# Kernel optimization log

Hardware: AMD Instinct MI355X
Metric: run time of the kernel (lower is better)

## Reference

```python
import jax, jax.numpy as jnp
import numpy as np

N = 64    # input_size (number of causal nodes)
H = 512   # hidden_size
M = 64    # mediate_size
B = 1024  # batched derivative evaluations (original processes one (1,N) state at a time)


def setup_inputs() -> dict:
    key = jax.random.key(0)
    ks = jax.random.split(key, 8)
    s = lambda fan_in: 1.0 / np.sqrt(fan_in)
    x = jax.random.normal(ks[0], (B, N), dtype=jnp.float32)
    # stacked per-node weights (one set per node i in 0..N-1)
    W1 = jax.random.uniform(ks[1], (N, H, N), jnp.float32, -s(N), s(N))        # net_1 layer 1, no bias
    W2 = jax.random.uniform(ks[2], (N, M, H), jnp.float32, -s(H), s(H))        # net_1 layer 2, no bias
    W3 = jax.random.uniform(ks[3], (N, H, M + N), jnp.float32, -s(M + N), s(M + N))  # net_3 layer 1
    b3 = jax.random.uniform(ks[4], (N, H), jnp.float32, -s(M + N), s(M + N))
    W4 = jax.random.uniform(ks[5], (N, H), jnp.float32, -s(H), s(H))           # net_3 layer 2 (out dim 1)
    b4 = jax.random.uniform(ks[6], (N,), jnp.float32, -s(H), s(H))
    return {"x": x, "W1": W1, "W2": W2, "W3": W3, "b3": b3, "W4": W4, "b4": b4}


def reference(x, W1, W2, W3, b3, W4, b4):
    # Faithful DAG-case CausalDerivative.forward, batched over B states and
    # grouped over the N per-node MLPs (replacing N python-loop iterations).
    eye = jnp.eye(N, dtype=x.dtype)
    inputs_1 = x[:, None, :] * (1.0 - eye)          # (B, N, N): node i sees all-but-own value
    inputs_2 = x[:, None, :] * eye                  # (B, N, N): node i sees only own value
    h1 = jax.nn.relu(jnp.einsum('bni,nhi->bnh', inputs_1, W1))   # (B, N, H)
    r1 = jax.nn.relu(jnp.einsum('bnh,nmh->bnm', h1, W2))         # (B, N, M)
    rep3 = jnp.concatenate([r1, inputs_2], axis=-1)              # (B, N, M+N)
    h3 = jax.nn.relu(jnp.einsum('bnk,nhk->bnh', rep3, W3) + b3)  # (B, N, H)
    out = jax.nn.relu(jnp.einsum('bnh,nh->bn', h3, W4) + b4)     # (B, N) derivatives
    return out
```

## Files before the change

### kernel.cpp

```cpp
#include <hip/hip_runtime.h>

#define NN 64
#define HH 512

typedef _Float16 h8 __attribute__((ext_vector_type(8)));
typedef float    fx4 __attribute__((ext_vector_type(4)));

#define MFMA __builtin_amdgcn_mfma_f32_16x16x32_f16

#define WS_NEEDED 12713984ull

typedef __attribute__((address_space(1))) const unsigned int gu32;
typedef __attribute__((address_space(3))) unsigned int       lu32;

__device__ __forceinline__ void gld16(const void* g, void* l) {
    __builtin_amdgcn_global_load_lds((gu32*)g, (lu32*)l, 16, 0, 0);
}

__device__ __forceinline__ h8 cvt8(const float* __restrict__ s) {
    float4 a = *(const float4*)s, b = *(const float4*)(s + 4);
    h8 h;
    h[0]=(_Float16)a.x; h[1]=(_Float16)a.y; h[2]=(_Float16)a.z; h[3]=(_Float16)a.w;
    h[4]=(_Float16)b.x; h[5]=(_Float16)b.y; h[6]=(_Float16)b.z; h[7]=(_Float16)b.w;
    return h;
}

__global__ __launch_bounds__(256)
void cvt_frag(const float* __restrict__ W1, const float* __restrict__ W2,
              const float* __restrict__ W3, char* __restrict__ ws)
{
    const int g    = blockIdx.x * 256 + threadIdx.x;
    const int n    = g >> 12;
    const int c    = (g >> 9) & 7;
    const int ks   = (g >> 8) & 1;
    const int nt   = (g >> 6) & 3;
    const int l    = g & 63;
    const int pos  = l & 15;
    const int quad = l >> 4;

    _Float16* o1 = (_Float16*)ws;
    _Float16* o2 = o1 + 2097152;
    _Float16* o3 = o2 + 2097152;
    float*    oc = (float*)(ws + 12582912);

    {
        const float* s = W1 + (size_t)n * 32768
                            + (size_t)(c * 64 + nt * 16 + pos) * 64
                            + ks * 32 + quad * 8;
        *(h8*)(o1 + (size_t)g * 8) = cvt8(s);
    }
    {
        const float* s = W2 + (size_t)n * 32768
                            + (size_t)(nt * 16 + pos) * 512
                            + c * 64 + ks * 32 + quad * 8;
        *(h8*)(o2 + (size_t)g * 8) = cvt8(s);
    }
    {
        const float* s = W3 + (size_t)n * 65536
                            + (size_t)(c * 64 + nt * 16 + pos) * 128
                            + ks * 32 + quad * 8;
        *(h8*)(o3 + (size_t)g * 8) = cvt8(s);
    }
    if (g < 32768) {
        const int n3 = g >> 9;
        const int h3 = g & 511;
        oc[g] = W3[(size_t)n3 * 65536 + (size_t)h3 * 128 + 64 + n3];
    }
}

__global__ __launch_bounds__(256, 2)
void causal_mfma5(const float* __restrict__ x, const char* __restrict__ ws,
                  const float* __restrict__ b3, const float* __restrict__ W4,
                  const float* __restrict__ b4, float* __restrict__ out)
{
    __shared__ __align__(16) char smem[57856];
    _Float16* w1b  = (_Float16*)smem;
    _Float16* w2b  = w1b + 8192;
    _Float16* priv = w2b + 8192;
    float*    w3cs = (float*)(smem + 51200);
    float*    b3s  = w3cs + 512;
    float*    w4s  = b3s + 512;
    float*    xns  = w4s + 512;

    const int tid  = threadIdx.x;
    const int bid  = blockIdx.x;
    const int n    = bid & 63;
    const int tile = bid >> 6;
    const int lane = tid & 63;
    const int pos  = lane & 15;
    const int quad = lane >> 4;
    const int wv   = __builtin_amdgcn_readfirstlane(tid >> 6);
    const int row0 = tile * 128;
    const int wrow = wv << 5;

    const _Float16* W1f  = (const _Float16*)ws + (size_t)n * 32768;
    const _Float16* W2f  = (const _Float16*)ws + 2097152 + (size_t)n * 32768;
    const _Float16* W3f  = (const _Float16*)ws + 4194304 + (size_t)n * 32768;
    const float*    w3cp = (const float*)(ws + 12582912) + n * 512;

    {
        const _Float16* s1 = W1f + wv * 1024 + lane * 8;
        gld16(s1,       w1b + wv * 1024);
        gld16(s1 + 512, w1b + wv * 1024 + 512);
        const _Float16* s2 = W2f + wv * 1024 + lane * 8;
        gld16(s2,       w2b + wv * 1024);
        gld16(s2 + 512, w2b + wv * 1024 + 512);
    }
    #pragma unroll
    for (int k = 0; k < 2; ++k) {
        const int h = tid + k * 256;
        w3cs[h] = w3cp[h];
        b3s[h]  = b3[n * HH + h];
        w4s[h]  = W4[n * HH + h];
    }
    if (tid < 128) xns[tid] = x[(size_t)(row0 + tid) * NN + n];

    h8 aX[2][2];
    #pragma unroll
    for (int mt = 0; mt < 2; ++mt)
        #pragma unroll
        for (int ks = 0; ks < 2; ++ks) {
            const float* p = x + (size_t)(row0 + wrow + mt * 16 + pos) * NN + ks * 32 + quad * 8;
            float4 a = *(const float4*)p, bq = *(const float4*)(p + 4);
            float v[8] = {a.x, a.y, a.z, a.w, bq.x, bq.y, bq.z, bq.w};
            const int base = ks * 32 + quad * 8;
            #pragma unroll
            for (int j = 0; j < 8; ++j) if (base + j == n) v[j] = 0.f;
            h8 h;
            #pragma unroll
            for (int j = 0; j < 8; ++j) h[j] = (_Float16)v[j];
            aX[mt][ks] = h;
        }
    __syncthreads();

    _Float16* P = priv + wv * 2304;

    fx4 acc2[2][4] = {};
    for (int c = 0; c < 8; ++c) {
        const int cb = c & 1;
        if (c < 7) {
            const _Float16* s1 = W1f + (c + 1) * 4096 + wv * 1024 + lane * 8;
            gld16(s1,       w1b + (cb ^ 1) * 4096 + wv * 1024);
            gld16(s1 + 512, w1b + (cb ^ 1) * 4096 + wv * 1024 + 512);
            const _Float16* s2 = W2f + (c + 1) * 4096 + wv * 1024 + lane * 8;
            gld16(s2,       w2b + (cb ^ 1) * 4096 + wv * 1024);
            gld16(s2 + 512, w2b + (cb ^ 1) * 4096 + wv * 1024 + 512);
        } else {
            const _Float16* s3 = W3f + wv * 1024 + lane * 8;
            gld16(s3,       w1b + wv * 1024);
            gld16(s3 + 512, w1b + wv * 1024 + 512);
        }
        const h8* F1 = (const h8*)(w1b + cb * 4096);
        fx4 accA[2][4] = {};
        #pragma unroll
        for (int ks = 0; ks < 2; ++ks)
            #pragma unroll
            for (int nt = 0; nt < 4; ++nt) {
                h8 bf = F1[(ks * 4 + nt) * 64 + lane];
                accA[0][nt] = MFMA(aX[0][ks], bf, accA[0][nt], 0, 0, 0);
                accA[1][nt] = MFMA(aX[1][ks], bf, accA[1][nt], 0, 0, 0);
            }
        #pragma unroll
        for (int mt = 0; mt < 2; ++mt)
            #pragma unroll
            for (int nt = 0; nt < 4; ++nt)
                #pragma unroll
                for (int r = 0; r < 4; ++r)
                    P[(mt * 16 + quad * 4 + r) * 72 + nt * 16 + pos] =
                        (_Float16)fmaxf(accA[mt][nt][r], 0.f);
        h8 aH[2][2];
        #pragma unroll
        for (int mt = 0; mt < 2; ++mt)
            #pragma unroll
            for (int ks = 0; ks < 2; ++ks)
                aH[mt][ks] = *(const h8*)(P + (mt * 16 + pos) * 72 + ks * 32 + quad * 8);
        const h8* F2 = (const h8*)(w2b + cb * 4096);
        #pragma unroll
        for (int ks = 0; ks < 2; ++ks)
            #pragma unroll
            for (int cm = 0; cm < 4; ++cm) {
                h8 bf = F2[(ks * 4 + cm) * 64 + lane];
                acc2[0][cm] = MFMA(aH[0][ks], bf, acc2[0][cm], 0, 0, 0);
                acc2[1][cm] = MFMA(aH[1][ks], bf, acc2[1][cm], 0, 0, 0);
            }
        __syncthreads();
    }

    #pragma unroll
    for (int mt = 0; mt < 2; ++mt)
        #pragma unroll
        for (int cm = 0; cm < 4; ++cm)
            #pragma unroll
            for (int r = 0; r < 4; ++r)
                P[(mt * 16 + quad * 4 + r) * 72 + cm * 16 + pos] =
                    (_Float16)fmaxf(acc2[mt][cm][r], 0.f);
    h8 aR[2][2];
    #pragma unroll
    for (int mt = 0; mt < 2; ++mt)
        #pragma unroll
        for (int ks = 0; ks < 2; ++ks)
            aR[mt][ks] = *(const h8*)(P + (mt * 16 + pos) * 72 + ks * 32 + quad * 8);
    h8 af3[2];
    #pragma unroll
    for (int mt = 0; mt < 2; ++mt) {
        h8 h;
        #pragma unroll
        for (int j = 0; j < 8; ++j) h[j] = (_Float16)0.f;
        if (quad == 0) { h[0] = (_Float16)xns[wrow + mt * 16 + pos]; h[1] = (_Float16)1.f; }
        af3[mt] = h;
    }

    float o[2][4] = {};
    for (int c = 0; c < 8; ++c) {
        const int cb = c & 1;
        const int hc = c << 6;
        if (c < 7) {
            const _Float16* s3 = W3f + (c + 1) * 4096 + wv * 1024 + lane * 8;
            gld16(s3,       w1b + (cb ^ 1) * 4096 + wv * 1024);
            gld16(s3 + 512, w1b + (cb ^ 1) * 4096 + wv * 1024 + 512);
        }
        const h8* F3 = (const h8*)(w1b + cb * 4096);
        fx4 acc3[2][4] = {};
        #pragma unroll
        for (int ks = 0; ks < 2; ++ks)
            #pragma unroll
            for (int nt = 0; nt < 4; ++nt) {
                h8 bf = F3[(ks * 4 + nt) * 64 + lane];
                acc3[0][nt] = MFMA(aR[0][ks], bf, acc3[0][nt], 0, 0, 0);
                acc3[1][nt] = MFMA(aR[1][ks], bf, acc3[1][nt], 0, 0, 0);
            }
        #pragma unroll
        for (int nt = 0; nt < 4; ++nt) {
            h8 bf3;
            #pragma unroll
            for (int j = 0; j < 8; ++j) bf3[j] = (_Float16)0.f;
            if (quad == 0) {
                const int h = hc + nt * 16 + pos;
                bf3[0] = (_Float16)w3cs[h];
                bf3[1] = (_Float16)b3s[h];
            }
            acc3[0][nt] = MFMA(af3[0], bf3, acc3[0][nt], 0, 0, 0);
            acc3[1][nt] = MFMA(af3[1], bf3, acc3[1][nt], 0, 0, 0);
        }
        #pragma unroll
        for (int nt = 0; nt < 4; ++nt) {
            const float w4v = w4s[hc + nt * 16 + pos];
            #pragma unroll
            for (int mt = 0; mt < 2; ++mt)
                #pragma unroll
                for (int r = 0; r < 4; ++r)
                    o[mt][r] = fmaf(fmaxf(acc3[mt][nt][r], 0.f), w4v, o[mt][r]);
        }
        __syncthreads();
    }

    #pragma unroll
    for (int m = 1; m < 16; m <<= 1)
        #pragma unroll
        for (int mt = 0; mt < 2; ++mt)
            #pragma unroll
            for (int r = 0; r < 4; ++r)
                o[mt][r] += __shfl_xor(o[mt][r], m, 64);

    if (pos == 0) {
        const float bb = b4[n];
        #pragma unroll
        for (int mt = 0; mt < 2; ++mt)
            #pragma unroll
            for (int r = 0; r < 4; ++r) {
                const int row = row0 + wrow + mt * 16 + quad * 4 + r;
                out[(size_t)row * 64 + n] = fmaxf(o[mt][r] + bb, 0.f);
            }
    }
}

__device__ __forceinline__ void cvt_store16(_Float16* d, const float4* p) {
    h8 h0, h1;
    h0[0]=(_Float16)p[0].x; h0[1]=(_Float16)p[0].y; h0[2]=(_Float16)p[0].z; h0[3]=(_Float16)p[0].w;
    h0[4]=(_Float16)p[1].x; h0[5]=(_Float16)p[1].y; h0[6]=(_Float16)p[1].z; h0[7]=(_Float16)p[1].w;
    h1[0]=(_Float16)p[2].x; h1[1]=(_Float16)p[2].y; h1[2]=(_Float16)p[2].z; h1[3]=(_Float16)p[2].w;
    h1[4]=(_Float16)p[3].x; h1[5]=(_Float16)p[3].y; h1[6]=(_Float16)p[3].z; h1[7]=(_Float16)p[3].w;
    *(h8*)d = h0; *((h8*)d + 1) = h1;
}

__global__ __launch_bounds__(256, 2)
void causal_mfma3(const float* __restrict__ x,  const float* __restrict__ W1,
                  const float* __restrict__ W2, const float* __restrict__ W3,
                  const float* __restrict__ b3, const float* __restrict__ W4,
                  const float* __restrict__ b4, float* __restrict__ out)
{
    __shared__ __align__(16) char smem[61952];
    _Float16* W1c  = (_Float16*)smem;
    _Float16* W2c  = W1c + 2 * 4608;
    _Float16* priv = W2c + 2 * 4608;
    float*    w3cs = (float*)(smem + 55296);
    float*    b3s  = w3cs + 512;
    float*    w4s  = b3s + 512;
    float*    xns  = w4s + 512;

    const int tid  = threadIdx.x;
    const int bid  = blockIdx.x;
    const int n    = bid & 63;
    const int tile = bid >> 6;
    const int lane = tid & 63;
    const int pos  = lane & 15;
    const int quad = lane >> 4;
    const int wv   = __builtin_amdgcn_readfirstlane(tid >> 6);
    const int row0 = tile * 128;
    const int wrow = wv << 5;

    const float* W1n = W1 + (size_t)n * HH * NN;
    const float* W2n = W2 + (size_t)n * NN * HH;
    const float* W3n = W3 + (size_t)n * HH * 128;

    const int trow = tid >> 2;
    const int tcol = (tid & 3) << 4;

    {
        float4 p1[4], p2[4];
        #pragma unroll
        for (int q = 0; q < 4; ++q) p1[q] = *(const float4*)(W1n + trow * 64 + tcol + q * 4);
        #pragma unroll
        for (int q = 0; q < 4; ++q) p2[q] = *(const float4*)(W2n + (size_t)trow * HH + tcol + q * 4);
        #pragma unroll
        for (int k = 0; k < 2; ++k) {
            const int h = tid + k * 256;
            w3cs[h] = W3n[(size_t)h * 128 + 64 + n];
            b3s[h]  = b3[n * HH + h];
            w4s[h]  = W4[n * HH + h];
        }
        if (tid < 128) xns[tid] = x[(size_t)(row0 + tid) * NN + n];
        cvt_store16(W1c + trow * 72 + tcol, p1);
        cvt_store16(W2c + trow * 72 + tcol, p2);
    }

    h8 aX[2][2];
    #pragma unroll
    for (int mt = 0; mt < 2; ++mt)
        #pragma unroll
        for (int ks = 0; ks < 2; ++ks) {
            const float* p = x + (size_t)(row0 + wrow + mt * 16 + pos) * NN + ks * 32 + quad * 8;
            float4 a = *(const float4*)p, bq = *(const float4*)(p + 4);
            float v[8] = {a.x, a.y, a.z, a.w, bq.x, bq.y, bq.z, bq.w};
            const int base = ks * 32 + quad * 8;
            #pragma unroll
            for (int j = 0; j < 8; ++j) if (base + j == n) v[j] = 0.f;
            h8 h;
            #pragma unroll
            for (int j = 0; j < 8; ++j) h[j] = (_Float16)v[j];
            aX[mt][ks] = h;
        }
    __syncthreads();

    _Float16* P = priv + wv * 2304;

    fx4 acc2[2][4] = {};
    for (int c = 0; c < 8; ++c) {
        const int cb = c & 1;
// ... 77 lines not shown
    }
    __syncthreads();

    float o[2][4] = {};
    for (int c = 0; c < 8; ++c) {
        const int cb = c & 1;
        const int hc = c << 6;
        float4 p3[4];
        if (c < 7) {
            #pragma unroll
            for (int q = 0; q < 4; ++q)
                p3[q] = *(const float4*)(W3n + (size_t)(hc + 64 + trow) * 128 + tcol + q * 4);
        }
        const _Float16* W3L = W1c + cb * 4608;
        fx4 acc3[2][4] = {};
        #pragma unroll
        for (int ks = 0; ks < 2; ++ks)
            #pragma unroll
            for (int nt = 0; nt < 4; ++nt) {
                h8 bf = *(const h8*)(W3L + (nt * 16 + pos) * 72 + ks * 32 + quad * 8);
                acc3[0][nt] = MFMA(aR[0][ks], bf, acc3[0][nt], 0, 0, 0);
                acc3[1][nt] = MFMA(aR[1][ks], bf, acc3[1][nt], 0, 0, 0);
            }
        #pragma unroll
        for (int nt = 0; nt < 4; ++nt) {
            h8 bf3;
            #pragma unroll
            for (int j = 0; j < 8; ++j) bf3[j] = (_Float16)0.f;
            if (quad == 0) {
                const int h = hc + nt * 16 + pos;
                bf3[0] = (_Float16)w3cs[h];
                bf3[1] = (_Float16)b3s[h];
            }
            acc3[0][nt] = MFMA(af3[0], bf3, acc3[0][nt], 0, 0, 0);
            acc3[1][nt] = MFMA(af3[1], bf3, acc3[1][nt], 0, 0, 0);
        }
        #pragma unroll
        for (int nt = 0; nt < 4; ++nt) {
            const float w4v = w4s[hc + nt * 16 + pos];
            #pragma unroll
            for (int mt = 0; mt < 2; ++mt)
                #pragma unroll
                for (int r = 0; r < 4; ++r)
                    o[mt][r] = fmaf(fmaxf(acc3[mt][nt][r], 0.f), w4v, o[mt][r]);
        }
        if (c < 7) cvt_store16(W1c + (cb ^ 1) * 4608 + trow * 72 + tcol, p3);
        __syncthreads();
    }

    #pragma unroll
    for (int m = 1; m < 16; m <<= 1)
        #pragma unroll
        for (int mt = 0; mt < 2; ++mt)
            #pragma unroll
            for (int r = 0; r < 4; ++r)
                o[mt][r] += __shfl_xor(o[mt][r], m, 64);

    if (pos == 0) {
        const float bb = b4[n];
        #pragma unroll
        for (int mt = 0; mt < 2; ++mt)
            #pragma unroll
            for (int r = 0; r < 4; ++r) {
                const int row = row0 + wrow + mt * 16 + quad * 4 + r;
                out[(size_t)row * 64 + n] = fmaxf(o[mt][r] + bb, 0.f);
            }
    }
}

extern "C" void kernel_launch(void* const* d_in, const int* in_sizes, int n_in,
                              void* d_out, int out_size, void* d_ws, size_t ws_size,
                              hipStream_t stream)
{
    const float* x  = (const float*)d_in[0];
    const float* W1 = (const float*)d_in[1];
    const float* W2 = (const float*)d_in[2];
    const float* W3 = (const float*)d_in[3];
    const float* b3 = (const float*)d_in[4];
    const float* W4 = (const float*)d_in[5];
    const float* b4 = (const float*)d_in[6];
    float* out = (float*)d_out;

    if (d_ws != nullptr && ws_size >= WS_NEEDED) {
        hipLaunchKernelGGL(cvt_frag, dim3(1024), dim3(256), 0, stream,
                           W1, W2, W3, (char*)d_ws);
        hipLaunchKernelGGL(causal_mfma5, dim3(512), dim3(256), 0, stream,
                           x, (const char*)d_ws, b3, W4, b4, out);
    } else {
        hipLaunchKernelGGL(causal_mfma3, dim3(512), dim3(256), 0, stream,
                           x, W1, W2, W3, b3, W4, b4, out);
    }
}
```

Baseline: 112.7 us.

## Fuse weight conversion into main kernel using cooperative grid sync

Merges the separate fp32-to-fp16 weight fragment conversion kernel into the main MFMA kernel. Each block converts its own slice of the weights to workspace, then all blocks meet at a cooperative grid-wide barrier before reading the converted fragments. This removes one kernel launch and its gap, at the cost of a grid barrier and a dependency on 512 blocks being co-resident. If the cooperative launch fails, the code falls back to the old two-kernel path.

```diff
diff --git a/kernel.cpp b/kernel.cpp
--- a/kernel.cpp
+++ b/kernel.cpp
@@ -1,4 +1,7 @@
 #include <hip/hip_runtime.h>
+#include <hip/hip_cooperative_groups.h>
+
+namespace cg = cooperative_groups;
 
 #define NN 64
 #define HH 512
@@ -25,53 +28,36 @@
     return h;
 }
 
-__global__ __launch_bounds__(256)
-void cvt_frag(const float* __restrict__ W1, const float* __restrict__ W2,
-              const float* __restrict__ W3, char* __restrict__ ws)
+__device__ __forceinline__ void cvt_slab16(const float* __restrict__ s,
+                                           _Float16* __restrict__ dst,
+                                           int rr, int c0)
 {
-    const int g    = blockIdx.x * 256 + threadIdx.x;
-    const int n    = g >> 12;
-    const int c    = (g >> 9) & 7;
-    const int ks   = (g >> 8) & 1;
-    const int nt   = (g >> 6) & 3;
-    const int l    = g & 63;
-    const int pos  = l & 15;
-    const int quad = l >> 4;
-
-    _Float16* o1 = (_Float16*)ws;
-    _Float16* o2 = o1 + 2097152;
-    _Float16* o3 = o2 + 2097152;
-    float*    oc = (float*)(ws + 12582912);
-
-    {
-        const float* s = W1 + (size_t)n * 32768
-                            + (size_t)(c * 64 + nt * 16 + pos) * 64
-                            + ks * 32 + quad * 8;
-        *(h8*)(o1 + (size_t)g * 8) = cvt8(s);
-    }
-    {
-        const float* s = W2 + (size_t)n * 32768
-                            + (size_t)(nt * 16 + pos) * 512
-                            + c * 64 + ks * 32 + quad * 8;
-        *(h8*)(o2 + (size_t)g * 8) = cvt8(s);
-    }
-    {
-        const float* s = W3 + (size_t)n * 65536
-                            + (size_t)(c * 64 + nt * 16 + pos) * 128
-                            + ks * 32 + quad * 8;
-        *(h8*)(o3 + (size_t)g * 8) = cvt8(s);
-    }
-    if (g < 32768) {
-        const int n3 = g >> 9;
-        const int h3 = g & 511;
-        oc[g] = W3[(size_t)n3 * 65536 + (size_t)h3 * 128 + 64 + n3];
+    const int nt  = rr >> 4;
+    const int pos = rr & 15;
+    float4 q[4];
+    #pragma unroll
+    for (int qq = 0; qq < 4; ++qq) q[qq] = *(const float4*)(s + qq * 4);
+    #pragma unroll
+    for (int g2 = 0; g2 < 2; ++g2) {
+        const int cg   = c0 + g2 * 8;
+        const int ks   = cg >> 5;
+        const int quad = (cg & 31) >> 3;
+        h8 h;
+        h[0]=(_Float16)q[g2*2].x;   h[1]=(_Float16)q[g2*2].y;
+        h[2]=(_Float16)q[g2*2].z;   h[3]=(_Float16)q[g2*2].w;
+        h[4]=(_Float16)q[g2*2+1].x; h[5]=(_Float16)q[g2*2+1].y;
+        h[6]=(_Float16)q[g2*2+1].z; h[7]=(_Float16)q[g2*2+1].w;
+        const int w = (ks * 4 + nt) * 64 + quad * 16 + pos;
+        *(h8*)(dst + w * 8) = h;
     }
 }
 
 __global__ __launch_bounds__(256, 2)
-void causal_mfma5(const float* __restrict__ x, const char* __restrict__ ws,
+void causal_fused(const float* __restrict__ x,  const float* __restrict__ W1,
+                  const float* __restrict__ W2, const float* __restrict__ W3,
                   const float* __restrict__ b3, const float* __restrict__ W4,
-                  const float* __restrict__ b4, float* __restrict__ out)
+                  const float* __restrict__ b4, char* __restrict__ ws,
+                  float* __restrict__ out)
 {
     __shared__ __align__(16) char smem[57856];
     _Float16* w1b  = (_Float16*)smem;
@@ -93,10 +79,30 @@
     const int row0 = tile * 128;
     const int wrow = wv << 5;
 
-    const _Float16* W1f  = (const _Float16*)ws + (size_t)n * 32768;
-    const _Float16* W2f  = (const _Float16*)ws + 2097152 + (size_t)n * 32768;
-    const _Float16* W3f  = (const _Float16*)ws + 4194304 + (size_t)n * 32768;
-    const float*    w3cp = (const float*)(ws + 12582912) + n * 512;
+    _Float16* o1 = (_Float16*)ws;
+    _Float16* o2 = o1 + 2097152;
+    _Float16* o3 = o2 + 2097152;
+    float*    oc = (float*)(ws + 12582912);
+
+    {
+        const int rr = tid >> 2;
+        const int c0 = (tid & 3) << 4;
+        cvt_slab16(W1 + (size_t)n * 32768 + (size_t)(tile * 64 + rr) * 64 + c0,
+                   o1 + (size_t)n * 32768 + tile * 4096, rr, c0);
+        cvt_slab16(W2 + (size_t)n * 32768 + (size_t)rr * 512 + tile * 64 + c0,
+                   o2 + (size_t)n * 32768 + tile * 4096, rr, c0);
+        cvt_slab16(W3 + (size_t)n * 65536 + (size_t)(tile * 64 + rr) * 128 + c0,
+                   o3 + (size_t)n * 32768 + tile * 4096, rr, c0);
+        if (tid < 64)
+            oc[n * 512 + tile * 64 + tid] =
+                W3[(size_t)n * 65536 + (size_t)(tile * 64 + tid) * 128 + 64 + n];
+    }
+    cg::this_grid().sync();
+
+    const _Float16* W1f  = o1 + (size_t)n * 32768;
+    const _Float16* W2f  = o2 + (size_t)n * 32768;
+    const _Float16* W3f  = o3 + (size_t)n * 32768;
+    const float*    w3cp = oc + n * 512;
 
     {
         const _Float16* s1 = W1f + wv * 1024 + lane * 8;
@@ -274,6 +280,255 @@
     }
 }
 
+__global__ __launch_bounds__(256)
+void cvt_frag(const float* __restrict__ W1, const float* __restrict__ W2,
+              const float* __restrict__ W3, char* __restrict__ ws)
+{
+    const int g    = blockIdx.x * 256 + threadIdx.x;
+    const int n    = g >> 12;
+    const int c    = (g >> 9) & 7;
+    const int ks   = (g >> 8) & 1;
+    const int nt   = (g >> 6) & 3;
+    const int l    = g & 63;
+    const int pos  = l & 15;
+    const int quad = l >> 4;
+
+    _Float16* o1 = (_Float16*)ws;
+    _Float16* o2 = o1 + 2097152;
+    _Float16* o3 = o2 + 2097152;
+    float*    oc = (float*)(ws + 12582912);
+
+    {
+        const float* s = W1 + (size_t)n * 32768
+                            + (size_t)(c * 64 + nt * 16 + pos) * 64
+                            + ks * 32 + quad * 8;
+        *(h8*)(o1 + (size_t)g * 8) = cvt8(s);
+    }
+    {
+        const float* s = W2 + (size_t)n * 32768
+                            + (size_t)(nt * 16 + pos) * 512
+                            + c * 64 + ks * 32 + quad * 8;
+        *(h8*)(o2 + (size_t)g * 8) = cvt8(s);
+    }
+    {
+        const float* s = W3 + (size_t)n * 65536
+                            + (size_t)(c * 64 + nt * 16 + pos) * 128
+                            + ks * 32 + quad * 8;
+        *(h8*)(o3 + (size_t)g * 8) = cvt8(s);
+    }
+    if (g < 32768) {
+        const int n3 = g >> 9;
+        const int h3 = g & 511;
+        oc[g] = W3[(size_t)n3 * 65536 + (size_t)h3 * 128 + 64 + n3];
+    }
+}
+
+__global__ __launch_bounds__(256, 2)
+void causal_mfma5(const float* __restrict__ x, const char* __restrict__ ws,
+                  const float* __restrict__ b3, const float* __restrict__ W4,
+                  const float* __restrict__ b4, float* __restrict__ out)
+{
+    __shared__ __align__(16) char smem[57856];
+    _Float16* w1b  = (_Float16*)smem;
+    _Float16* w2b  = w1b + 8192;
+    _Float16* priv = w2b + 8192;
+    float*    w3cs = (float*)(smem + 51200);
+    float*    b3s  = w3cs + 512;
+    float*    w4s  = b3s + 512;
+    float*    xns  = w4s + 512;
+
+    const int tid  = threadIdx.x;
+    const int bid  = blockIdx.x;
+    const int n    = bid & 63;
+    const int tile = bid >> 6;
+    const int lane = tid & 63;
+    const int pos  = lane & 15;
+    const int quad = lane >> 4;
+    const int wv   = __builtin_amdgcn_readfirstlane(tid >> 6);
+    const int row0 = tile * 128;
+    const int wrow = wv << 5;
+
+    const _Float16* W1f  = (const _Float16*)ws + (size_t)n * 32768;
+    const _Float16* W2f  = (const _Float16*)ws + 2097152 + (size_t)n * 32768;
+    const _Float16* W3f  = (const _Float16*)ws + 4194304 + (size_t)n * 32768;
+    const float*    w3cp = (const float*)(ws + 12582912) + n * 512;
+
+    {
+        const _Float16* s1 = W1f + wv * 1024 + lane * 8;
+        gld16(s1,       w1b + wv * 1024);
+        gld16(s1 + 512, w1b + wv * 1024 + 512);
+        const _Float16* s2 = W2f + wv * 1024 + lane * 8;
+        gld16(s2,       w2b + wv * 1024);
+        gld16(s2 + 512, w2b + wv * 1024 + 512);
+    }
+    #pragma unroll
+    for (int k = 0; k < 2; ++k) {
+        const int h = tid + k * 256;
+        w3cs[h] = w3cp[h];
+        b3s[h]  = b3[n * HH + h];
+        w4s[h]  = W4[n * HH + h];
+    }
+    if (tid < 128) xns[tid] = x[(size_t)(row0 + tid) * NN + n];
+
+    h8 aX[2][2];
+    #pragma unroll
+    for (int mt = 0; mt < 2; ++mt)
+        #pragma unroll
+        for (int ks = 0; ks < 2; ++ks) {
+            const float* p = x + (size_t)(row0 + wrow + mt * 16 + pos) * NN + ks * 32 + quad * 8;
+            float4 a = *(const float4*)p, bq = *(const float4*)(p + 4);
+            float v[8] = {a.x, a.y, a.z, a.w, bq.x, bq.y, bq.z, bq.w};
+            const int base = ks * 32 + quad * 8;
+            #pragma unroll
+            for (int j = 0; j < 8; ++j) if (base + j == n) v[j] = 0.f;
+            h8 h;
+            #pragma unroll
+            for (int j = 0; j < 8; ++j) h[j] = (_Float16)v[j];
+            aX[mt][ks] = h;
+        }
+    __syncthreads();
+
+    _Float16* P = priv + wv * 2304;
+
+    fx4 acc2[2][4] = {};
+    for (int c = 0; c < 8; ++c) {
+        const int cb = c & 1;
+        if (c < 7) {
+            const _Float16* s1 = W1f + (c + 1) * 4096 + wv * 1024 + lane * 8;
+            gld16(s1,       w1b + (cb ^ 1) * 4096 + wv * 1024);
+            gld16(s1 + 512, w1b + (cb ^ 1) * 4096 + wv * 1024 + 512);
+            const _Float16* s2 = W2f + (c + 1) * 4096 + wv * 1024 + lane * 8;
+            gld16(s2,       w2b + (cb ^ 1) * 4096 + wv * 1024);
+            gld16(s2 + 512, w2b + (cb ^ 1) * 4096 + wv * 1024 + 512);
+        } else {
+            const _Float16* s3 = W3f + wv * 1024 + lane * 8;
+            gld16(s3,       w1b + wv * 1024);
+            gld16(s3 + 512, w1b + wv * 1024 + 512);
+        }
+        const h8* F1 = (const h8*)(w1b + cb * 4096);
+        fx4 accA[2][4] = {};
+        #pragma unroll
+        for (int ks = 0; ks < 2; ++ks)
+            #pragma unroll
+            for (int nt = 0; nt < 4; ++nt) {
+                h8 bf = F1[(ks * 4 + nt) * 64 + lane];
+                accA[0][nt] = MFMA(aX[0][ks], bf, accA[0][nt], 0, 0, 0);
+                accA[1][nt] = MFMA(aX[1][ks], bf, accA[1][nt], 0, 0, 0);
+            }
+        #pragma unroll
+        for (int mt = 0; mt < 2; ++mt)
+            #pragma unroll
+            for (int nt = 0; nt < 4; ++nt)
+                #pragma unroll
+                for (int r = 0; r < 4; ++r)
+                    P[(mt * 16 + quad * 4 + r) * 72 + nt * 16 + pos] =
+                        (_Float16)fmaxf(accA[mt][nt][r], 0.f);
+        h8 aH[2][2];
+        #pragma unroll
+        for (int mt = 0; mt < 2; ++mt)
+            #pragma unroll
+            for (int ks = 0; ks < 2; ++ks)
+                aH[mt][ks] = *(const h8*)(P + (mt * 16 + pos) * 72 + ks * 32 + quad * 8);
+        const h8* F2 = (const h8*)(w2b + cb * 4096);
+        #pragma unroll
+        for (int ks = 0; ks < 2; ++ks)
+            #pragma unroll
+            for (int cm = 0; cm < 4; ++cm) {
+                h8 bf = F2[(ks * 4 + cm) * 64 + lane];
+                acc2[0][cm] = MFMA(aH[0][ks], bf, acc2[0][cm], 0, 0, 0);
+                acc2[1][cm] = MFMA(aH[1][ks], bf, acc2[1][cm], 0, 0, 0);
+            }
+        __syncthreads();
+    }
+
+    #pragma unroll
+    for (int mt = 0; mt < 2; ++mt)
+        #pragma unroll
+        for (int cm = 0; cm < 4; ++cm)
+            #pragma unroll
+            for (int r = 0; r < 4; ++r)
+                P[(mt * 16 + quad * 4 + r) * 72 + cm * 16 + pos] =
+                    (_Float16)fmaxf(acc2[mt][cm][r], 0.f);
+    h8 aR[2][2];
+    #pragma unroll
+    for (int mt = 0; mt < 2; ++mt)
+        #pragma unroll
+        for (int ks = 0; ks < 2; ++ks)
+            aR[mt][ks] = *(const h8*)(P + (mt * 16 + pos) * 72 + ks * 32 + quad * 8);
+    h8 af3[2];
+    #pragma unroll
+    for (int mt = 0; mt < 2; ++mt) {
+        h8 h;
+        #pragma unroll
+        for (int j = 0; j < 8; ++j) h[j] = (_Float16)0.f;
+        if (quad == 0) { h[0] = (_Float16)xns[wrow + mt * 16 + pos]; h[1] = (_Float16)1.f; }
+        af3[mt] = h;
+    }
+
+    float o[2][4] = {};
+    for (int c = 0; c < 8; ++c) {
+        const int cb = c & 1;
+        const int hc = c << 6;
+        if (c < 7) {
+            const _Float16* s3 = W3f + (c + 1) * 4096 + wv * 1024 + lane * 8;
+            gld16(s3,       w1b + (cb ^ 1) * 4096 + wv * 1024);
+            gld16(s3 + 512, w1b + (cb ^ 1) * 4096 + wv * 1024 + 512);
+        }
+        const h8* F3 = (const h8*)(w1b + cb * 4096);
+        fx4 acc3[2][4] = {};
+        #pragma unroll
+        for (int ks = 0; ks < 2; ++ks)
+            #pragma unroll
+            for (int nt = 0; nt < 4; ++nt) {
+                h8 bf = F3[(ks * 4 + nt) * 64 + lane];
+                acc3[0][nt] = MFMA(aR[0][ks], bf, acc3[0][nt], 0, 0, 0);
+                acc3[1][nt] = MFMA(aR[1][ks], bf, acc3[1][nt], 0, 0, 0);
+            }
+        #pragma unroll
+        for (int nt = 0; nt < 4; ++nt) {
+            h8 bf3;
+            #pragma unroll
+            for (int j = 0; j < 8; ++j) bf3[j] = (_Float16)0.f;
+            if (quad == 0) {
+                const int h = hc + nt * 16 + pos;
+                bf3[0] = (_Float16)w3cs[h];
+                bf3[1] = (_Float16)b3s[h];
+            }
+            acc3[0][nt] = MFMA(af3[0], bf3, acc3[0][nt], 0, 0, 0);
+            acc3[1][nt] = MFMA(af3[1], bf3, acc3[1][nt], 0, 0, 0);
+        }
+        #pragma unroll
+        for (int nt = 0; nt < 4; ++nt) {
+            const float w4v = w4s[hc + nt * 16 + pos];
+            #pragma unroll
+            for (int mt = 0; mt < 2; ++mt)
+                #pragma unroll
+                for (int r = 0; r < 4; ++r)
+                    o[mt][r] = fmaf(fmaxf(acc3[mt][nt][r], 0.f), w4v, o[mt][r]);
+        }
+        __syncthreads();
+    }
+
+    #pragma unroll
+    for (int m = 1; m < 16; m <<= 1)
+        #pragma unroll
+        for (int mt = 0; mt < 2; ++mt)
+            #pragma unroll
+            for (int r = 0; r < 4; ++r)
+                o[mt][r] += __shfl_xor(o[mt][r], m, 64);
+
+    if (pos == 0) {
+        const float bb = b4[n];
+        #pragma unroll
+        for (int mt = 0; mt < 2; ++mt)
+            #pragma unroll
+            for (int r = 0; r < 4; ++r) {
+                const int row = row0 + wrow + mt * 16 + quad * 4 + r;
+                out[(size_t)row * 64 + n] = fmaxf(o[mt][r] + bb, 0.f);
+            }
+    }
+}
+
 __device__ __forceinline__ void cvt_store16(_Float16* d, const float4* p) {
     h8 h0, h1;
     h0[0]=(_Float16)p[0].x; h0[1]=(_Float16)p[0].y; h0[2]=(_Float16)p[0].z; h0[3]=(_Float16)p[0].w;
@@ -517,10 +772,18 @@
     float* out = (float*)d_out;
 
     if (d_ws != nullptr && ws_size >= WS_NEEDED) {
-        hipLaunchKernelGGL(cvt_frag, dim3(1024), dim3(256), 0, stream,
-                           W1, W2, W3, (char*)d_ws);
-        hipLaunchKernelGGL(causal_mfma5, dim3(512), dim3(256), 0, stream,
-                           x, (const char*)d_ws, b3, W4, b4, out);
+        char* ws = (char*)d_ws;
+        void* args[] = {(void*)&x, (void*)&W1, (void*)&W2, (void*)&W3,
+                        (void*)&b3, (void*)&W4, (void*)&b4, (void*)&ws, (void*)&out};
+        hipError_t err = hipLaunchCooperativeKernel(
+            reinterpret_cast<void*>(causal_fused), dim3(512), dim3(256),
+            args, 0, stream);
+        if (err != hipSuccess) {
+            hipLaunchKernelGGL(cvt_frag, dim3(1024), dim3(256), 0, stream,
+                               W1, W2, W3, ws);
+            hipLaunchKernelGGL(causal_mfma5, dim3(512), dim3(256), 0, stream,
+                               x, (const char*)ws, b3, W4, b4, out);
+        }
     } else {
         hipLaunchKernelGGL(causal_mfma3, dim3(512), dim3(256), 0, stream,
                            x, W1, W2, W3, b3, W4, b4, out);
```

After: 178.6 us. +58.6%, slower.

## Load weight fragments directly into registers and swap MFMA operand order

Applied to the files above, without the earlier changes.

The main kernel no longer stages W1/W2/W3 fp16 fragments through shared memory with global_load_lds and per-chunk barriers. Each wave now loads its fragments straight from global (L2) into registers, double-buffered in registers, and removes most __syncthreads. MFMA operands are swapped so the accumulator comes out transposed, which allows vectorized h4 stores to LDS and a cheaper final reduction with only two shuffles. The conversion kernel's block-to-node mapping is also permuted. Risks are higher register pressure from holding 24+ h8 fragments per thread and redundant global loads across the four waves.

```diff
diff --git a/kernel.cpp b/kernel.cpp
--- a/kernel.cpp
+++ b/kernel.cpp
@@ -4,18 +4,12 @@
 #define HH 512
 
 typedef _Float16 h8 __attribute__((ext_vector_type(8)));
+typedef _Float16 h4 __attribute__((ext_vector_type(4)));
 typedef float    fx4 __attribute__((ext_vector_type(4)));
 
 #define MFMA __builtin_amdgcn_mfma_f32_16x16x32_f16
 
 #define WS_NEEDED 12713984ull
-
-typedef __attribute__((address_space(1))) const unsigned int gu32;
-typedef __attribute__((address_space(3))) unsigned int       lu32;
-
-__device__ __forceinline__ void gld16(const void* g, void* l) {
-    __builtin_amdgcn_global_load_lds((gu32*)g, (lu32*)l, 16, 0, 0);
-}
 
 __device__ __forceinline__ h8 cvt8(const float* __restrict__ s) {
     float4 a = *(const float4*)s, b = *(const float4*)(s + 4);
@@ -29,7 +23,10 @@
 void cvt_frag(const float* __restrict__ W1, const float* __restrict__ W2,
               const float* __restrict__ W3, char* __restrict__ ws)
 {
-    const int g    = blockIdx.x * 256 + threadIdx.x;
+    const int bid  = blockIdx.x;
+    const int nb   = bid & 63;
+    const int sub  = bid >> 6;
+    const int g    = nb * 4096 + sub * 256 + threadIdx.x;
     const int n    = g >> 12;
     const int c    = (g >> 9) & 7;
     const int ks   = (g >> 8) & 1;
@@ -69,15 +66,13 @@
 }
 
 __global__ __launch_bounds__(256, 2)
-void causal_mfma5(const float* __restrict__ x, const char* __restrict__ ws,
+void causal_mfma6(const float* __restrict__ x, const char* __restrict__ ws,
                   const float* __restrict__ b3, const float* __restrict__ W4,
                   const float* __restrict__ b4, float* __restrict__ out)
 {
-    __shared__ __align__(16) char smem[57856];
-    _Float16* w1b  = (_Float16*)smem;
-    _Float16* w2b  = w1b + 8192;
-    _Float16* priv = w2b + 8192;
-    float*    w3cs = (float*)(smem + 51200);
+    __shared__ __align__(16) char smem[25088];
+    _Float16* priv = (_Float16*)smem;
+    float*    w3cs = (float*)(smem + 18432);
     float*    b3s  = w3cs + 512;
     float*    w4s  = b3s + 512;
     float*    xns  = w4s + 512;
@@ -93,19 +88,11 @@
     const int row0 = tile * 128;
     const int wrow = wv << 5;
 
-    const _Float16* W1f  = (const _Float16*)ws + (size_t)n * 32768;
-    const _Float16* W2f  = (const _Float16*)ws + 2097152 + (size_t)n * 32768;
-    const _Float16* W3f  = (const _Float16*)ws + 4194304 + (size_t)n * 32768;
-    const float*    w3cp = (const float*)(ws + 12582912) + n * 512;
-
-    {
-        const _Float16* s1 = W1f + wv * 1024 + lane * 8;
-        gld16(s1,       w1b + wv * 1024);
-        gld16(s1 + 512, w1b + wv * 1024 + 512);
-        const _Float16* s2 = W2f + wv * 1024 + lane * 8;
-        gld16(s2,       w2b + wv * 1024);
-        gld16(s2 + 512, w2b + wv * 1024 + 512);
-    }
+    const h8* W1f = (const h8*)ws + (size_t)n * 4096;
+    const h8* W2f = (const h8*)(ws + 4194304) + (size_t)n * 4096;
+    const h8* W3f = (const h8*)(ws + 8388608) + (size_t)n * 4096;
+    const float* w3cp = (const float*)(ws + 12582912) + n * 512;
+
     #pragma unroll
     for (int k = 0; k < 2; ++k) {
         const int h = tid + k * 256;
@@ -131,69 +118,66 @@
             for (int j = 0; j < 8; ++j) h[j] = (_Float16)v[j];
             aX[mt][ks] = h;
         }
-    __syncthreads();
 
     _Float16* P = priv + wv * 2304;
 
     fx4 acc2[2][4] = {};
-    for (int c = 0; c < 8; ++c) {
-        const int cb = c & 1;
+    h8 f1a[8], f1b[8], f2[8];
+
+    #pragma unroll
+    for (int t = 0; t < 8; ++t) f1a[t] = W1f[t * 64 + lane];
+
+    auto bodyAB = [&](h8 (&cur1)[8], h8 (&nxt1)[8], int c) {
         if (c < 7) {
-            const _Float16* s1 = W1f + (c + 1) * 4096 + wv * 1024 + lane * 8;
-            gld16(s1,       w1b + (cb ^ 1) * 4096 + wv * 1024);
-            gld16(s1 + 512, w1b + (cb ^ 1) * 4096 + wv * 1024 + 512);
-            const _Float16* s2 = W2f + (c + 1) * 4096 + wv * 1024 + lane * 8;
-            gld16(s2,       w2b + (cb ^ 1) * 4096 + wv * 1024);
-            gld16(s2 + 512, w2b + (cb ^ 1) * 4096 + wv * 1024 + 512);
-        } else {
-            const _Float16* s3 = W3f + wv * 1024 + lane * 8;
-            gld16(s3,       w1b + wv * 1024);
-            gld16(s3 + 512, w1b + wv * 1024 + 512);
-        }
-        const h8* F1 = (const h8*)(w1b + cb * 4096);
+            #pragma unroll
+            for (int t = 0; t < 8; ++t) nxt1[t] = W1f[((c + 1) * 8 + t) * 64 + lane];
+        }
+        #pragma unroll
+        for (int t = 0; t < 8; ++t) f2[t] = W2f[(c * 8 + t) * 64 + lane];
         fx4 accA[2][4] = {};
         #pragma unroll
         for (int ks = 0; ks < 2; ++ks)
             #pragma unroll
             for (int nt = 0; nt < 4; ++nt) {
-                h8 bf = F1[(ks * 4 + nt) * 64 + lane];
-                accA[0][nt] = MFMA(aX[0][ks], bf, accA[0][nt], 0, 0, 0);
-                accA[1][nt] = MFMA(aX[1][ks], bf, accA[1][nt], 0, 0, 0);
+                accA[0][nt] = MFMA(cur1[ks * 4 + nt], aX[0][ks], accA[0][nt], 0, 0, 0);
+                accA[1][nt] = MFMA(cur1[ks * 4 + nt], aX[1][ks], accA[1][nt], 0, 0, 0);
             }
         #pragma unroll
         for (int mt = 0; mt < 2; ++mt)
             #pragma unroll
-            for (int nt = 0; nt < 4; ++nt)
+            for (int nt = 0; nt < 4; ++nt) {
+                h4 w;
                 #pragma unroll
-                for (int r = 0; r < 4; ++r)
-                    P[(mt * 16 + quad * 4 + r) * 72 + nt * 16 + pos] =
-                        (_Float16)fmaxf(accA[mt][nt][r], 0.f);
+                for (int r = 0; r < 4; ++r) w[r] = (_Float16)fmaxf(accA[mt][nt][r], 0.f);
+                *(h4*)(P + (mt * 16 + pos) * 72 + nt * 16 + quad * 4) = w;
+            }
         h8 aH[2][2];
         #pragma unroll
         for (int mt = 0; mt < 2; ++mt)
             #pragma unroll
             for (int ks = 0; ks < 2; ++ks)
                 aH[mt][ks] = *(const h8*)(P + (mt * 16 + pos) * 72 + ks * 32 + quad * 8);
-        const h8* F2 = (const h8*)(w2b + cb * 4096);
         #pragma unroll
         for (int ks = 0; ks < 2; ++ks)
             #pragma unroll
             for (int cm = 0; cm < 4; ++cm) {
-                h8 bf = F2[(ks * 4 + cm) * 64 + lane];
-                acc2[0][cm] = MFMA(aH[0][ks], bf, acc2[0][cm], 0, 0, 0);
-                acc2[1][cm] = MFMA(aH[1][ks], bf, acc2[1][cm], 0, 0, 0);
-            }
-        __syncthreads();
-    }
+                acc2[0][cm] = MFMA(f2[ks * 4 + cm], aH[0][ks], acc2[0][cm], 0, 0, 0);
+                acc2[1][cm] = MFMA(f2[ks * 4 + cm], aH[1][ks], acc2[1][cm], 0, 0, 0);
+            }
+    };
+    for (int c = 0; c < 8; c += 2) { bodyAB(f1a, f1b, c); bodyAB(f1b, f1a, c + 1); }
 
     #pragma unroll
     for (int mt = 0; mt < 2; ++mt)
         #pragma unroll
-        for (int cm = 0; cm < 4; ++cm)
-            #pragma unroll
-            for (int r = 0; r < 4; ++r)
-                P[(mt * 16 + quad * 4 + r) * 72 + cm * 16 + pos] =
-                    (_Float16)fmaxf(acc2[mt][cm][r], 0.f);
+        for (int cm = 0; cm < 4; ++cm) {
+            h4 w;
+            #pragma unroll
+            for (int r = 0; r < 4; ++r) w[r] = (_Float16)fmaxf(acc2[mt][cm][r], 0.f);
+            *(h4*)(P + (mt * 16 + pos) * 72 + cm * 16 + quad * 4) = w;
+        }
+    __syncthreads();
+
     h8 aR[2][2];
     #pragma unroll
     for (int mt = 0; mt < 2; ++mt)
@@ -210,24 +194,24 @@
         af3[mt] = h;
     }
 
-    float o[2][4] = {};
-    for (int c = 0; c < 8; ++c) {
-        const int cb = c & 1;
+    float o[2] = {0.f, 0.f};
+    h8 f3a[8], f3b[8];
+    #pragma unroll
+    for (int t = 0; t < 8; ++t) f3a[t] = W3f[t * 64 + lane];
+
+    auto bodyC = [&](h8 (&cur3)[8], h8 (&nxt3)[8], int c) {
         const int hc = c << 6;
         if (c < 7) {
-            const _Float16* s3 = W3f + (c + 1) * 4096 + wv * 1024 + lane * 8;
-            gld16(s3,       w1b + (cb ^ 1) * 4096 + wv * 1024);
-            gld16(s3 + 512, w1b + (cb ^ 1) * 4096 + wv * 1024 + 512);
-        }
-        const h8* F3 = (const h8*)(w1b + cb * 4096);
+            #pragma unroll
+            for (int t = 0; t < 8; ++t) nxt3[t] = W3f[((c + 1) * 8 + t) * 64 + lane];
+        }
         fx4 acc3[2][4] = {};
         #pragma unroll
         for (int ks = 0; ks < 2; ++ks)
             #pragma unroll
             for (int nt = 0; nt < 4; ++nt) {
-                h8 bf = F3[(ks * 4 + nt) * 64 + lane];
-                acc3[0][nt] = MFMA(aR[0][ks], bf, acc3[0][nt], 0, 0, 0);
-                acc3[1][nt] = MFMA(aR[1][ks], bf, acc3[1][nt], 0, 0, 0);
+                acc3[0][nt] = MFMA(cur3[ks * 4 + nt], aR[0][ks], acc3[0][nt], 0, 0, 0);
+                acc3[1][nt] = MFMA(cur3[ks * 4 + nt], aR[1][ks], acc3[1][nt], 0, 0, 0);
             }
         #pragma unroll
         for (int nt = 0; nt < 4; ++nt) {
@@ -239,38 +223,33 @@
                 bf3[0] = (_Float16)w3cs[h];
                 bf3[1] = (_Float16)b3s[h];
             }
-            acc3[0][nt] = MFMA(af3[0], bf3, acc3[0][nt], 0, 0, 0);
-            acc3[1][nt] = MFMA(af3[1], bf3, acc3[1][nt], 0, 0, 0);
+            acc3[0][nt] = MFMA(bf3, af3[0], acc3[0][nt], 0, 0, 0);
+            acc3[1][nt] = MFMA(bf3, af3[1], acc3[1][nt], 0, 0, 0);
         }
         #pragma unroll
         for (int nt = 0; nt < 4; ++nt) {
-            const float w4v = w4s[hc + nt * 16 + pos];
+            const fx4 w4v = *(const fx4*)(w4s + hc + nt * 16 + quad * 4);
             #pragma unroll
             for (int mt = 0; mt < 2; ++mt)
                 #pragma unroll
                 for (int r = 0; r < 4; ++r)
-                    o[mt][r] = fmaf(fmaxf(acc3[mt][nt][r], 0.f), w4v, o[mt][r]);
-        }
-        __syncthreads();
-    }
-
-    #pragma unroll
-    for (int m = 1; m < 16; m <<= 1)
-        #pragma unroll
-        for (int mt = 0; mt < 2; ++mt)
-            #pragma unroll
-            for (int r = 0; r < 4; ++r)
-                o[mt][r] += __shfl_xor(o[mt][r], m, 64);
-
-    if (pos == 0) {
+                    o[mt] = fmaf(fmaxf(acc3[mt][nt][r], 0.f), w4v[r], o[mt]);
+        }
+    };
+    for (int c = 0; c < 8; c += 2) { bodyC(f3a, f3b, c); bodyC(f3b, f3a, c + 1); }
+
+    #pragma unroll
+    for (int mt = 0; mt < 2; ++mt) {
+        o[mt] += __shfl_xor(o[mt], 16, 64);
+        o[mt] += __shfl_xor(o[mt], 32, 64);
+    }
+    if (quad == 0) {
         const float bb = b4[n];
         #pragma unroll
-        for (int mt = 0; mt < 2; ++mt)
-            #pragma unroll
-            for (int r = 0; r < 4; ++r) {
-                const int row = row0 + wrow + mt * 16 + quad * 4 + r;
-                out[(size_t)row * 64 + n] = fmaxf(o[mt][r] + bb, 0.f);
-            }
+        for (int mt = 0; mt < 2; ++mt) {
+            const int row = row0 + wrow + mt * 16 + pos;
+            out[(size_t)row * 64 + n] = fmaxf(o[mt] + bb, 0.f);
+        }
     }
 }
 
@@ -519,7 +498,7 @@
     if (d_ws != nullptr && ws_size >= WS_NEEDED) {
         hipLaunchKernelGGL(cvt_frag, dim3(1024), dim3(256), 0, stream,
                            W1, W2, W3, (char*)d_ws);
-        hipLaunchKernelGGL(causal_mfma5, dim3(512), dim3(256), 0, stream,
+        hipLaunchKernelGGL(causal_mfma6, dim3(512), dim3(256), 0, stream,
                            x, (const char*)d_ws, b3, W4, b4, out);
     } else {
         hipLaunchKernelGGL(causal_mfma3, dim3(512), dim3(256), 0, stream,
```

Result: no change. 113.0 us (+0.3%).

## Halve row tile, swap MFMA operands, read W2 fragments directly from global

Applied to the files above, without the earlier changes.

The main kernel now processes 64 rows per block instead of 128 and launches twice as many blocks. W2 fragments are loaded straight into registers from global memory rather than staged through shared memory, and the W3 column and bias are packed as fp16 pairs. Together these cut shared memory to about 30KB and allow four blocks per CU. MFMA operands are transposed so weights are the A operand, which lets the ReLU results be written to shared memory as 4-wide vectors and shortens the final reduction to two shuffles. The conversion kernel's block-to-node mapping is also permuted. The cost is twice the weight traffic per row and global-latency W2 loads inside the loop.

```diff
diff --git a/kernel.cpp b/kernel.cpp
--- a/kernel.cpp
+++ b/kernel.cpp
@@ -4,6 +4,7 @@
 #define HH 512
 
 typedef _Float16 h8 __attribute__((ext_vector_type(8)));
+typedef _Float16 h4 __attribute__((ext_vector_type(4)));
 typedef float    fx4 __attribute__((ext_vector_type(4)));
 
 #define MFMA __builtin_amdgcn_mfma_f32_16x16x32_f16
@@ -29,7 +30,10 @@
 void cvt_frag(const float* __restrict__ W1, const float* __restrict__ W2,
               const float* __restrict__ W3, char* __restrict__ ws)
 {
-    const int g    = blockIdx.x * 256 + threadIdx.x;
+    const int bid  = blockIdx.x;
+    const int nb   = bid & 63;
+    const int sub  = bid >> 6;
+    const int g    = nb * 4096 + sub * 256 + threadIdx.x;
     const int n    = g >> 12;
     const int c    = (g >> 9) & 7;
     const int ks   = (g >> 8) & 1;
@@ -68,19 +72,17 @@
     }
 }
 
-__global__ __launch_bounds__(256, 2)
-void causal_mfma5(const float* __restrict__ x, const char* __restrict__ ws,
+__global__ __launch_bounds__(256, 4)
+void causal_mfma7(const float* __restrict__ x, const char* __restrict__ ws,
                   const float* __restrict__ b3, const float* __restrict__ W4,
                   const float* __restrict__ b4, float* __restrict__ out)
 {
-    __shared__ __align__(16) char smem[57856];
+    __shared__ __align__(16) char smem[29952];
     _Float16* w1b  = (_Float16*)smem;
-    _Float16* w2b  = w1b + 8192;
-    _Float16* priv = w2b + 8192;
-    float*    w3cs = (float*)(smem + 51200);
-    float*    b3s  = w3cs + 512;
-    float*    w4s  = b3s + 512;
-    float*    xns  = w4s + 512;
+    _Float16* priv = w1b + 8192;
+    _Float16* wb3h = (_Float16*)(smem + 25600);
+    float*    w4s  = (float*)(smem + 27648);
+    float*    xns  = (float*)(smem + 29696);
 
     const int tid  = threadIdx.x;
     const int bid  = blockIdx.x;
@@ -90,145 +92,119 @@
     const int pos  = lane & 15;
     const int quad = lane >> 4;
     const int wv   = __builtin_amdgcn_readfirstlane(tid >> 6);
-    const int row0 = tile * 128;
-    const int wrow = wv << 5;
-
-    const _Float16* W1f  = (const _Float16*)ws + (size_t)n * 32768;
-    const _Float16* W2f  = (const _Float16*)ws + 2097152 + (size_t)n * 32768;
-    const _Float16* W3f  = (const _Float16*)ws + 4194304 + (size_t)n * 32768;
-    const float*    w3cp = (const float*)(ws + 12582912) + n * 512;
-
-    {
-        const _Float16* s1 = W1f + wv * 1024 + lane * 8;
+    const int row0 = tile * 64;
+    const int wrow = wv << 4;
+
+    const _Float16* W1h = (const _Float16*)ws + (size_t)n * 32768;
+    const h8*       W2f = (const h8*)(ws + 4194304) + (size_t)n * 4096;
+    const _Float16* W3h = (const _Float16*)(ws + 8388608) + (size_t)n * 32768;
+    const float*   w3cp = (const float*)(ws + 12582912) + n * 512;
+
+    {
+        const _Float16* s1 = W1h + wv * 1024 + lane * 8;
         gld16(s1,       w1b + wv * 1024);
         gld16(s1 + 512, w1b + wv * 1024 + 512);
-        const _Float16* s2 = W2f + wv * 1024 + lane * 8;
-        gld16(s2,       w2b + wv * 1024);
-        gld16(s2 + 512, w2b + wv * 1024 + 512);
     }
     #pragma unroll
     for (int k = 0; k < 2; ++k) {
         const int h = tid + k * 256;
-        w3cs[h] = w3cp[h];
-        b3s[h]  = b3[n * HH + h];
-        w4s[h]  = W4[n * HH + h];
-    }
-    if (tid < 128) xns[tid] = x[(size_t)(row0 + tid) * NN + n];
-
-    h8 aX[2][2];
-    #pragma unroll
-    for (int mt = 0; mt < 2; ++mt)
-        #pragma unroll
-        for (int ks = 0; ks < 2; ++ks) {
-            const float* p = x + (size_t)(row0 + wrow + mt * 16 + pos) * NN + ks * 32 + quad * 8;
-            float4 a = *(const float4*)p, bq = *(const float4*)(p + 4);
-            float v[8] = {a.x, a.y, a.z, a.w, bq.x, bq.y, bq.z, bq.w};
-            const int base = ks * 32 + quad * 8;
-            #pragma unroll
-            for (int j = 0; j < 8; ++j) if (base + j == n) v[j] = 0.f;
-            h8 h;
-            #pragma unroll
-            for (int j = 0; j < 8; ++j) h[j] = (_Float16)v[j];
-            aX[mt][ks] = h;
-        }
+        wb3h[h * 2]     = (_Float16)w3cp[h];
+        wb3h[h * 2 + 1] = (_Float16)b3[n * HH + h];
+        w4s[h]          = W4[n * HH + h];
+    }
+    if (tid < 64) xns[tid] = x[(size_t)(row0 + tid) * NN + n];
+
+    h8 aX[2];
+    #pragma unroll
+    for (int ks = 0; ks < 2; ++ks) {
+        const float* p = x + (size_t)(row0 + wrow + pos) * NN + ks * 32 + quad * 8;
+        float4 a = *(const float4*)p, bq = *(const float4*)(p + 4);
+        float v[8] = {a.x, a.y, a.z, a.w, bq.x, bq.y, bq.z, bq.w};
+        const int base = ks * 32 + quad * 8;
+        #pragma unroll
+        for (int j = 0; j < 8; ++j) if (base + j == n) v[j] = 0.f;
+        h8 h;
+        #pragma unroll
+        for (int j = 0; j < 8; ++j) h[j] = (_Float16)v[j];
+        aX[ks] = h;
+    }
     __syncthreads();
 
-    _Float16* P = priv + wv * 2304;
-
-    fx4 acc2[2][4] = {};
+    _Float16* P = priv + wv * 1152;
+
+    fx4 acc2[4] = {};
     for (int c = 0; c < 8; ++c) {
         const int cb = c & 1;
         if (c < 7) {
-            const _Float16* s1 = W1f + (c + 1) * 4096 + wv * 1024 + lane * 8;
+            const _Float16* s1 = W1h + (c + 1) * 4096 + wv * 1024 + lane * 8;
             gld16(s1,       w1b + (cb ^ 1) * 4096 + wv * 1024);
             gld16(s1 + 512, w1b + (cb ^ 1) * 4096 + wv * 1024 + 512);
-            const _Float16* s2 = W2f + (c + 1) * 4096 + wv * 1024 + lane * 8;
-            gld16(s2,       w2b + (cb ^ 1) * 4096 + wv * 1024);
-            gld16(s2 + 512, w2b + (cb ^ 1) * 4096 + wv * 1024 + 512);
         } else {
-            const _Float16* s3 = W3f + wv * 1024 + lane * 8;
-            gld16(s3,       w1b + wv * 1024);
-            gld16(s3 + 512, w1b + wv * 1024 + 512);
-        }
+            const _Float16* s3 = W3h + wv * 1024 + lane * 8;
+            gld16(s3,       w1b + (cb ^ 1) * 4096 + wv * 1024);
+            gld16(s3 + 512, w1b + (cb ^ 1) * 4096 + wv * 1024 + 512);
+        }
+        h8 f2[8];
+        #pragma unroll
+        for (int t = 0; t < 8; ++t) f2[t] = W2f[(c * 8 + t) * 64 + lane];
         const h8* F1 = (const h8*)(w1b + cb * 4096);
-        fx4 accA[2][4] = {};
-        #pragma unroll
-        for (int ks = 0; ks < 2; ++ks)
-            #pragma unroll
-            for (int nt = 0; nt < 4; ++nt) {
-                h8 bf = F1[(ks * 4 + nt) * 64 + lane];
-                accA[0][nt] = MFMA(aX[0][ks], bf, accA[0][nt], 0, 0, 0);
-                accA[1][nt] = MFMA(aX[1][ks], bf, accA[1][nt], 0, 0, 0);
-            }
-        #pragma unroll
-        for (int mt = 0; mt < 2; ++mt)
+        fx4 accA[4] = {};
+        #pragma unroll
+        for (int ks = 0; ks < 2; ++ks)
             #pragma unroll
             for (int nt = 0; nt < 4; ++nt)
-                #pragma unroll
-                for (int r = 0; r < 4; ++r)
-                    P[(mt * 16 + quad * 4 + r) * 72 + nt * 16 + pos] =
-                        (_Float16)fmaxf(accA[mt][nt][r], 0.f);
-        h8 aH[2][2];
-        #pragma unroll
-        for (int mt = 0; mt < 2; ++mt)
-            #pragma unroll
-            for (int ks = 0; ks < 2; ++ks)
-                aH[mt][ks] = *(const h8*)(P + (mt * 16 + pos) * 72 + ks * 32 + quad * 8);
-        const h8* F2 = (const h8*)(w2b + cb * 4096);
-        #pragma unroll
-        for (int ks = 0; ks < 2; ++ks)
-            #pragma unroll
-            for (int cm = 0; cm < 4; ++cm) {
-                h8 bf = F2[(ks * 4 + cm) * 64 + lane];
-                acc2[0][cm] = MFMA(aH[0][ks], bf, acc2[0][cm], 0, 0, 0);
-                acc2[1][cm] = MFMA(aH[1][ks], bf, acc2[1][cm], 0, 0, 0);
-            }
+                accA[nt] = MFMA(F1[(ks * 4 + nt) * 64 + lane], aX[ks], accA[nt], 0, 0, 0);
+        #pragma unroll
+        for (int nt = 0; nt < 4; ++nt) {
+            h4 w;
+            #pragma unroll
+            for (int r = 0; r < 4; ++r) w[r] = (_Float16)fmaxf(accA[nt][r], 0.f);
+            *(h4*)(P + pos * 72 + nt * 16 + quad * 4) = w;
+        }
+        h8 aH[2];
+        #pragma unroll
+        for (int ks = 0; ks < 2; ++ks)
+            aH[ks] = *(const h8*)(P + pos * 72 + ks * 32 + quad * 8);
+        #pragma unroll
+        for (int ks = 0; ks < 2; ++ks)
+            #pragma unroll
+            for (int cm = 0; cm < 4; ++cm)
+                acc2[cm] = MFMA(f2[ks * 4 + cm], aH[ks], acc2[cm], 0, 0, 0);
         __syncthreads();
     }
 
     #pragma unroll
-    for (int mt = 0; mt < 2; ++mt)
-        #pragma unroll
-        for (int cm = 0; cm < 4; ++cm)
-            #pragma unroll
-            for (int r = 0; r < 4; ++r)
-                P[(mt * 16 + quad * 4 + r) * 72 + cm * 16 + pos] =
-                    (_Float16)fmaxf(acc2[mt][cm][r], 0.f);
-    h8 aR[2][2];
-    #pragma unroll
-    for (int mt = 0; mt < 2; ++mt)
-        #pragma unroll
-        for (int ks = 0; ks < 2; ++ks)
-            aR[mt][ks] = *(const h8*)(P + (mt * 16 + pos) * 72 + ks * 32 + quad * 8);
-    h8 af3[2];
-    #pragma unroll
-    for (int mt = 0; mt < 2; ++mt) {
-        h8 h;
-        #pragma unroll
-        for (int j = 0; j < 8; ++j) h[j] = (_Float16)0.f;
-        if (quad == 0) { h[0] = (_Float16)xns[wrow + mt * 16 + pos]; h[1] = (_Float16)1.f; }
-        af3[mt] = h;
-    }
-
-    float o[2][4] = {};
+    for (int cm = 0; cm < 4; ++cm) {
+        h4 w;
+        #pragma unroll
+        for (int r = 0; r < 4; ++r) w[r] = (_Float16)fmaxf(acc2[cm][r], 0.f);
+        *(h4*)(P + pos * 72 + cm * 16 + quad * 4) = w;
+    }
+    h8 aR[2];
+    #pragma unroll
+    for (int ks = 0; ks < 2; ++ks)
+        aR[ks] = *(const h8*)(P + pos * 72 + ks * 32 + quad * 8);
+    h8 af3;
+    #pragma unroll
+    for (int j = 0; j < 8; ++j) af3[j] = (_Float16)0.f;
+    if (quad == 0) { af3[0] = (_Float16)xns[wrow + pos]; af3[1] = (_Float16)1.f; }
+
+    float o = 0.f;
     for (int c = 0; c < 8; ++c) {
         const int cb = c & 1;
         const int hc = c << 6;
         if (c < 7) {
-            const _Float16* s3 = W3f + (c + 1) * 4096 + wv * 1024 + lane * 8;
+            const _Float16* s3 = W3h + (c + 1) * 4096 + wv * 1024 + lane * 8;
             gld16(s3,       w1b + (cb ^ 1) * 4096 + wv * 1024);
             gld16(s3 + 512, w1b + (cb ^ 1) * 4096 + wv * 1024 + 512);
         }
         const h8* F3 = (const h8*)(w1b + cb * 4096);
-        fx4 acc3[2][4] = {};
-        #pragma unroll
-        for (int ks = 0; ks < 2; ++ks)
-            #pragma unroll
-            for (int nt = 0; nt < 4; ++nt) {
-                h8 bf = F3[(ks * 4 + nt) * 64 + lane];
-                acc3[0][nt] = MFMA(aR[0][ks], bf, acc3[0][nt], 0, 0, 0);
-                acc3[1][nt] = MFMA(aR[1][ks], bf, acc3[1][nt], 0, 0, 0);
-            }
+        fx4 acc3[4] = {};
+        #pragma unroll
+        for (int ks = 0; ks < 2; ++ks)
+            #pragma unroll
+            for (int nt = 0; nt < 4; ++nt)
+                acc3[nt] = MFMA(F3[(ks * 4 + nt) * 64 + lane], aR[ks], acc3[nt], 0, 0, 0);
         #pragma unroll
         for (int nt = 0; nt < 4; ++nt) {
             h8 bf3;
@@ -236,41 +212,26 @@
             for (int j = 0; j < 8; ++j) bf3[j] = (_Float16)0.f;
             if (quad == 0) {
                 const int h = hc + nt * 16 + pos;
-                bf3[0] = (_Float16)w3cs[h];
-                bf3[1] = (_Float16)b3s[h];
-            }
-            acc3[0][nt] = MFMA(af3[0], bf3, acc3[0][nt], 0, 0, 0);
-            acc3[1][nt] = MFMA(af3[1], bf3, acc3[1][nt], 0, 0, 0);
+                bf3[0] = wb3h[h * 2];
+                bf3[1] = wb3h[h * 2 + 1];
+            }
+            acc3[nt] = MFMA(bf3, af3, acc3[nt], 0, 0, 0);
         }
         #pragma unroll
         for (int nt = 0; nt < 4; ++nt) {
-            const float w4v = w4s[hc + nt * 16 + pos];
-            #pragma unroll
-            for (int mt = 0; mt < 2; ++mt)
-                #pragma unroll
-                for (int r = 0; r < 4; ++r)
-                    o[mt][r] = fmaf(fmaxf(acc3[mt][nt][r], 0.f), w4v, o[mt][r]);
+            const fx4 w4v = *(const fx4*)(w4s + hc + nt * 16 + quad * 4);
+            #pragma unroll
+            for (int r = 0; r < 4; ++r)
+                o = fmaf(fmaxf(acc3[nt][r], 0.f), w4v[r], o);
         }
         __syncthreads();
     }
 
-    #pragma unroll
-    for (int m = 1; m < 16; m <<= 1)
-        #pragma unroll
-        for (int mt = 0; mt < 2; ++mt)
-            #pragma unroll
-            for (int r = 0; r < 4; ++r)
-                o[mt][r] += __shfl_xor(o[mt][r], m, 64);
-
-    if (pos == 0) {
-        const float bb = b4[n];
-        #pragma unroll
-        for (int mt = 0; mt < 2; ++mt)
-            #pragma unroll
-            for (int r = 0; r < 4; ++r) {
-                const int row = row0 + wrow + mt * 16 + quad * 4 + r;
-                out[(size_t)row * 64 + n] = fmaxf(o[mt][r] + bb, 0.f);
-            }
+    o += __shfl_xor(o, 16, 64);
+    o += __shfl_xor(o, 32, 64);
+    if (quad == 0) {
+        const int row = row0 + wrow + pos;
+        out[(size_t)row * 64 + n] = fmaxf(o + b4[n], 0.f);
     }
 }
 
@@ -519,7 +480,7 @@
     if (d_ws != nullptr && ws_size >= WS_NEEDED) {
         hipLaunchKernelGGL(cvt_frag, dim3(1024), dim3(256), 0, stream,
                            W1, W2, W3, (char*)d_ws);
-        hipLaunchKernelGGL(causal_mfma5, dim3(512), dim3(256), 0, stream,
+        hipLaunchKernelGGL(causal_mfma7, dim3(1024), dim3(256), 0, stream,
                            x, (const char*)d_ws, b3, W4, b4, out);
     } else {
         hipLaunchKernelGGL(causal_mfma3, dim3(512), dim3(256), 0, stream,
```

Measured after the change: 111.2 us. No clear change (-1.3%).
